# Optimization experiments

Hardware: AMD Instinct MI355X
Metric: run time of the kernel (lower is better)

## Reference

```python
import jax, jax.numpy as jnp
import numpy as np

SIGMA = 0.05  # gaussian bandwidth from the source


def _sqdist(a, b):
    # a: [B,N,D], b: [B,M,D] -> [B,N,M] squared euclidean distance
    a2 = jnp.sum(a * a, axis=-1)[:, :, None]
    b2 = jnp.sum(b * b, axis=-1)[:, None, :]
    return a2 + b2 - 2.0 * jnp.einsum('bnd,bmd->bnm', a, b)


def setup_inputs() -> dict:
    key = jax.random.key(0)
    k1, k2, k3, k4 = jax.random.split(key, 4)
    B, N, D = 2, 4096, 32
    points = jax.random.normal(k1, (B, N, 3), dtype=jnp.float32)
    pointfea1 = jax.random.normal(k2, (B, N, D), dtype=jnp.float32)
    pointfea2 = jax.random.normal(k3, (B, N, D), dtype=jnp.float32)
    weights = jax.random.uniform(k4, (B, N), dtype=jnp.float32) / N  # point-cloud mass weights
    return {"points": points, "pointfea1": pointfea1, "pointfea2": pointfea2, "weights": weights}


def reference(points, pointfea1, pointfea2, weights):
    # naive_corres: per-point spatial log-gaussian softmax vs feature log-softmax,
    # weighted squared difference, reduced over both pair axes -> [B]
    x = points / SIGMA
    point_loggauss = jax.nn.log_softmax(-_sqdist(x, x), axis=2)          # [B,N,N]
    fea_logsoftmax = jax.nn.log_softmax(-_sqdist(pointfea1, pointfea2), axis=2)  # [B,N,N]
    diff2 = (jnp.exp(point_loggauss) - jnp.exp(fea_logsoftmax)) ** 2
    l2_loss = jnp.sum(diff2 * weights[:, :, None], axis=2)  # sum over j
    return jnp.sum(l2_loss, axis=1)                          # sum over i -> [B]
```

## Files before the change

### kernel.cpp

```cpp
#include <hip/hip_runtime.h>

#define D    32
#define BLK  256
#define BLKP 64
#define NCH  16
#define SJ   128

#define LOG2E 1.44269504088896340736f

typedef short  short8  __attribute__((ext_vector_type(8)));
typedef float  floatx4 __attribute__((ext_vector_type(4)));
typedef float  v2f     __attribute__((ext_vector_type(2)));

__device__ __forceinline__ short f2bf(float v) {
    union { float f; unsigned u; } x; x.f = v;
    unsigned r = x.u + 0x7fffu + ((x.u >> 16) & 1u);
    return (short)(r >> 16);
}
__device__ __forceinline__ float bf2f(short h) {
    union { float f; unsigned u; } x;
    x.u = ((unsigned)(unsigned short)h) << 16;
    return x.f;
}
__device__ __forceinline__ float fast_exp2(float x) {
#if __has_builtin(__builtin_amdgcn_exp2f)
    return __builtin_amdgcn_exp2f(x);
#else
    return exp2f(x);
#endif
}

__global__ __launch_bounds__(BLKP) void precompute_kernel(
    const float* __restrict__ points,
    const float* __restrict__ fea1,
    const float* __restrict__ fea2,
    float4* __restrict__ xp,
    float* __restrict__ f1n,
    float* __restrict__ f2n,
    short* __restrict__ f2hi,
    short* __restrict__ f2lo,
    float* __restrict__ acc,
    float* __restrict__ out,
    int BN, int Bsz)
{
    int r = blockIdx.x * BLKP + threadIdx.x;
    if (r < Bsz) out[r] = 0.0f;
    if (r >= BN) return;
#pragma unroll
    for (int s = 0; s < 5; ++s) acc[s * BN + r] = 0.0f;

    const float s20 = 20.0f;
    float x = points[3*r+0] * s20;
    float y = points[3*r+1] * s20;
    float z = points[3*r+2] * s20;
    float4 v; v.x = x; v.y = y; v.z = z;
    v.w = (x*x + y*y + z*z) * LOG2E;
    xp[r] = v;

    const float4* p1 = (const float4*)(fea1 + (size_t)r * D);
    float n1 = 0.f;
#pragma unroll
    for (int k = 0; k < D/4; ++k) {
        float4 a = p1[k];
        n1 = fmaf(a.x,a.x, fmaf(a.y,a.y, fmaf(a.z,a.z, fmaf(a.w,a.w, n1))));
    }
    f1n[r] = n1 * LOG2E;

    const int t = r >> 4;
    const int m = r & 15;
    const float* p2 = fea2 + (size_t)r * D;
    float n2 = 0.f;
#pragma unroll
    for (int q = 0; q < 4; ++q) {
        float4 v0 = *(const float4*)(p2 + q*8);
        float4 v1 = *(const float4*)(p2 + q*8 + 4);
        float e[8] = {v0.x,v0.y,v0.z,v0.w,v1.x,v1.y,v1.z,v1.w};
        short8 h, l;
#pragma unroll
        for (int k = 0; k < 8; ++k) {
            n2 = fmaf(e[k], e[k], n2);
            short hh = f2bf(e[k]);
            h[k] = hh;
            l[k] = f2bf(e[k] - bf2f(hh));
        }
        size_t off = ((size_t)t * 64 + m + 16*q) * 8;
        *(short8*)&f2hi[off] = h;
        *(short8*)&f2lo[off] = l;
    }
    f2n[r] = n2 * LOG2E;
}

__global__ __launch_bounds__(BLK, 8) void pair_kernel(
    const float* __restrict__ fea1,
    const short* __restrict__ f2hi,
    const short* __restrict__ f2lo,
    const float4* __restrict__ xp,
    const float* __restrict__ f1n,
    const float* __restrict__ f2n,
    float* __restrict__ acc,
    int N, int BN)
{
    __shared__ __align__(16) short sHi[SJ * D];
    __shared__ __align__(16) short sLo[SJ * D];

    const int tid  = threadIdx.x;
    const int lane = tid & 63;
    const int wv   = tid >> 6;
    const int m    = lane & 15;
    const int q    = lane >> 4;

    const int ibpb  = N / 64;
    const int b     = blockIdx.x / ibpb;
    const int ibase = blockIdx.x * 64 + wv * 16;
    const int JCH   = N / NCH;
    const int jc0   = blockIdx.y * JCH;

    const float* f1p = fea1 + (size_t)(ibase + m) * D + q * 8;
    float4 bv0 = *(const float4*)(f1p);
    float4 bv1 = *(const float4*)(f1p + 4);
    float bf[8] = {bv0.x,bv0.y,bv0.z,bv0.w,bv1.x,bv1.y,bv1.z,bv1.w};
    short8 Bhi, Blo;
#pragma unroll
    for (int k = 0; k < 8; ++k) {
        short h = f2bf(bf[k]);
        Bhi[k] = h;
        Blo[k] = f2bf(bf[k] - bf2f(h));
    }

    const float L2 = 2.0f * LOG2E;
    float4 xi = xp[ibase + m];
    float xix = xi.x * L2, xiy = xi.y * L2, xiz = xi.z * L2;
    float mxiw = -xi.w;
    float nfi  = -f1n[ibase + m];

    v2f sAB = {0.f, 0.f};
    v2f s2  = {0.f, 0.f};
    float sab = 0.f;

    const short*  gHi  = f2hi + ((size_t)(b * N + jc0) >> 4) * 512;
    const short*  gLo  = f2lo + ((size_t)(b * N + jc0) >> 4) * 512;
    const float4* xpb  = xp  + (size_t)b * N + jc0;
    const float*  f2nb = f2n + (size_t)b * N + jc0;

    for (int s = 0; s < JCH; s += SJ) {
        const uint4* srcH = (const uint4*)(gHi + (size_t)(s >> 4) * 512);
        const uint4* srcL = (const uint4*)(gLo + (size_t)(s >> 4) * 512);
        uint4* dstH = (uint4*)sHi;
        uint4* dstL = (uint4*)sLo;
        dstH[tid]       = srcH[tid];
        dstH[tid + 256] = srcH[tid + 256];
        dstL[tid]       = srcL[tid];
        dstL[tid + 256] = srcL[tid + 256];
        __syncthreads();

        const float4* xps = xpb + s;
        const float*  fns = f2nb + s;

#pragma unroll 2
        for (int jt8 = 0; jt8 < SJ/16; ++jt8) {
            const short8 Ahi = *(const short8*)&sHi[(jt8 * 64 + lane) * 8];
            const short8 Alo = *(const short8*)&sLo[(jt8 * 64 + lane) * 8];
            floatx4 c = {0.f, 0.f, 0.f, 0.f};
            c = __builtin_amdgcn_mfma_f32_16x16x32_bf16(Ahi, Bhi, c, 0, 0, 0);
            c = __builtin_amdgcn_mfma_f32_16x16x32_bf16(Ahi, Blo, c, 0, 0, 0);
            c = __builtin_amdgcn_mfma_f32_16x16x32_bf16(Alo, Bhi, c, 0, 0, 0);
#pragma unroll
            for (int r = 0; r < 4; ++r) {
                int jl = jt8 * 16 + q * 4 + r;
                float4 xj = xps[jl];
                float bL = fmaf(c[r], L2, nfi - fns[jl]);
                float aL = fmaf(xiz, xj.z,
                             fmaf(xiy, xj.y,
                              fmaf(xix, xj.x, mxiw))) - xj.w;
                float ea = fast_exp2(aL);
                float eb = fast_exp2(bL);
                v2f e = {ea, eb};
                sAB += e;
                s2   = __builtin_elementwise_fma(e, e, s2);
                sab  = fmaf(ea, eb, sab);
            }
        }
        __syncthreads();
    }

    float vA = sAB.x, vB = sAB.y, v2a = s2.x, v2b = s2.y, vab = sab;
    vA  += __shfl_xor(vA, 16);  vA  += __shfl_xor(vA, 32);
    vB  += __shfl_xor(vB, 16);  vB  += __shfl_xor(vB, 32);
    v2a += __shfl_xor(v2a, 16); v2a += __shfl_xor(v2a, 32);
    v2b += __shfl_xor(v2b, 16); v2b += __shfl_xor(v2b, 32);
    vab += __shfl_xor(vab, 16); vab += __shfl_xor(vab, 32);

    if (lane < 16) {
        int row = ibase + lane;
        atomicAdd(&acc[0*BN + row], vA);
        atomicAdd(&acc[1*BN + row], v2a);
        atomicAdd(&acc[2*BN + row], vB);
        atomicAdd(&acc[3*BN + row], v2b);
        atomicAdd(&acc[4*BN + row], vab);
    }
}

__global__ __launch_bounds__(BLK) void finalize_kernel(
    const float* __restrict__ acc,
    const float* __restrict__ weights,
    float* __restrict__ out,
    int N, int BN)
{
    int row = blockIdx.x * BLK + threadIdx.x;
    int b   = (blockIdx.x * BLK) / N;

    float A   = acc[0*BN + row];
    float S2a = acc[1*BN + row];
    float Bt  = acc[2*BN + row];
    float S2b = acc[3*BN + row];
    float Sab = acc[4*BN + row];
    float invA = 1.0f / A;
    float invB = 1.0f / Bt;
    float val  = S2a*invA*invA - 2.0f*Sab*invA*invB + S2b*invB*invB;
    float sum  = weights[row] * val;

    __shared__ float red[BLK/64];
    for (int off = 32; off > 0; off >>= 1)
        sum += __shfl_down(sum, off);
    if ((threadIdx.x & 63) == 0) red[threadIdx.x >> 6] = sum;
    __syncthreads();
    if (threadIdx.x == 0) {
        float s = 0.f;
#pragma unroll
        for (int w = 0; w < BLK/64; ++w) s += red[w];
        atomicAdd(&out[b], s);
    }
}

extern "C" void kernel_launch(void* const* d_in, const int* in_sizes, int n_in,
                              void* d_out, int out_size, void* d_ws, size_t ws_size,
                              hipStream_t stream) {
    const float* points  = (const float*)d_in[0];
    const float* fea1    = (const float*)d_in[1];
    const float* fea2    = (const float*)d_in[2];
    const float* weights = (const float*)d_in[3];
    float* out = (float*)d_out;

    int B  = out_size;
    int BN = in_sizes[3];
    int N  = BN / B;

    float*  acc  = (float*)d_ws;
    float4* xp   = (float4*)((char*)d_ws + (size_t)5  * BN * 4);
    float*  f2n  = (float*)((char*)d_ws + (size_t)9  * BN * 4);
    float*  f1n  = (float*)((char*)d_ws + (size_t)10 * BN * 4);
    short*  f2hi = (short*)((char*)d_ws + (size_t)11 * BN * 4);
    short*  f2lo = f2hi + (size_t)BN * D;

    precompute_kernel<<<dim3((BN + BLKP - 1) / BLKP), dim3(BLKP), 0, stream>>>(
        points, fea1, fea2, xp, f1n, f2n, f2hi, f2lo, acc, out, BN, B);

    dim3 grid(BN / 64, NCH);
    pair_kernel<<<grid, dim3(BLK), 0, stream>>>(
        fea1, f2hi, f2lo, xp, f1n, f2n, acc, N, BN);

    finalize_kernel<<<dim3(BN / BLK), dim3(BLK), 0, stream>>>(acc, weights, out, N, BN);
}
```

Measured before the change: 92.29 us.

## Pack per-j point/norm data pairwise, stage in LDS, and use packed v2f math

Precompute now writes per-column x,y,z, negated squared norm and negated feature norm interleaved in pairs (12 floats per 2 columns). The pair kernel stages this into shared memory alongside the bf16 tiles. It then processes two columns at a time with 2-wide float vector FMAs, which can map to packed FP32 instructions. This replaces per-element global loads of xp and f2n inside the hot loop and halves the scalar FMA count, at the cost of extra LDS traffic and a sync-covered copy.

```diff
diff --git a/kernel.cpp b/kernel.cpp
--- a/kernel.cpp
+++ b/kernel.cpp
@@ -36,7 +36,7 @@
     const float* __restrict__ fea2,
     float4* __restrict__ xp,
     float* __restrict__ f1n,
-    float* __restrict__ f2n,
+    float* __restrict__ jpk,
     short* __restrict__ f2hi,
     short* __restrict__ f2lo,
     float* __restrict__ acc,
@@ -87,21 +87,28 @@
         *(short8*)&f2hi[off] = h;
         *(short8*)&f2lo[off] = l;
     }
-    f2n[r] = n2 * LOG2E;
+
+    float* jb = jpk + (size_t)(r >> 1) * 12 + (r & 1);
+    jb[0] = v.x;
+    jb[2] = v.y;
+    jb[4] = v.z;
+    jb[6] = -v.w;
+    jb[8] = -n2 * LOG2E;
 }
 
 __global__ __launch_bounds__(BLK, 8) void pair_kernel(
     const float* __restrict__ fea1,
     const short* __restrict__ f2hi,
     const short* __restrict__ f2lo,
+    const float* __restrict__ jpk,
     const float4* __restrict__ xp,
     const float* __restrict__ f1n,
-    const float* __restrict__ f2n,
     float* __restrict__ acc,
     int N, int BN)
 {
     __shared__ __align__(16) short sHi[SJ * D];
     __shared__ __align__(16) short sLo[SJ * D];
+    __shared__ __align__(16) float sJP[(SJ/2) * 12];
 
     const int tid  = threadIdx.x;
     const int lane = tid & 63;
@@ -129,32 +136,37 @@
 
     const float L2 = 2.0f * LOG2E;
     float4 xi = xp[ibase + m];
-    float xix = xi.x * L2, xiy = xi.y * L2, xiz = xi.z * L2;
-    float mxiw = -xi.w;
-    float nfi  = -f1n[ibase + m];
-
-    v2f sAB = {0.f, 0.f};
-    v2f s2  = {0.f, 0.f};
-    float sab = 0.f;
-
-    const short*  gHi  = f2hi + ((size_t)(b * N + jc0) >> 4) * 512;
-    const short*  gLo  = f2lo + ((size_t)(b * N + jc0) >> 4) * 512;
-    const float4* xpb  = xp  + (size_t)b * N + jc0;
-    const float*  f2nb = f2n + (size_t)b * N + jc0;
+    float nfi = -f1n[ibase + m];
+    v2f vxx2 = {xi.x * L2, xi.x * L2};
+    v2f vxy2 = {xi.y * L2, xi.y * L2};
+    v2f vxz2 = {xi.z * L2, xi.z * L2};
+    v2f vmw2 = {-xi.w, -xi.w};
+    v2f vnf2 = {nfi, nfi};
+    v2f vL2  = {L2, L2};
+
+    v2f sA2  = {0.f, 0.f};
+    v2f sB2  = {0.f, 0.f};
+    v2f s2a2 = {0.f, 0.f};
+    v2f s2b2 = {0.f, 0.f};
+    v2f sab2 = {0.f, 0.f};
+
+    const short* gHi = f2hi + ((size_t)(b * N + jc0) >> 4) * 512;
+    const short* gLo = f2lo + ((size_t)(b * N + jc0) >> 4) * 512;
+    const float* gJP = jpk  + ((size_t)(b * N + jc0) >> 1) * 12;
 
     for (int s = 0; s < JCH; s += SJ) {
         const uint4* srcH = (const uint4*)(gHi + (size_t)(s >> 4) * 512);
         const uint4* srcL = (const uint4*)(gLo + (size_t)(s >> 4) * 512);
+        const uint4* srcJ = (const uint4*)(gJP + (size_t)(s >> 1) * 12);
         uint4* dstH = (uint4*)sHi;
         uint4* dstL = (uint4*)sLo;
         dstH[tid]       = srcH[tid];
         dstH[tid + 256] = srcH[tid + 256];
         dstL[tid]       = srcL[tid];
         dstL[tid + 256] = srcL[tid + 256];
+        if (tid < (SJ/2) * 12 * 4 / 16)
+            ((uint4*)sJP)[tid] = srcJ[tid];
         __syncthreads();
-
-        const float4* xps = xpb + s;
-        const float*  fns = f2nb + s;
 
 #pragma unroll 2
         for (int jt8 = 0; jt8 < SJ/16; ++jt8) {
@@ -165,25 +177,39 @@
             c = __builtin_amdgcn_mfma_f32_16x16x32_bf16(Ahi, Blo, c, 0, 0, 0);
             c = __builtin_amdgcn_mfma_f32_16x16x32_bf16(Alo, Bhi, c, 0, 0, 0);
 #pragma unroll
-            for (int r = 0; r < 4; ++r) {
-                int jl = jt8 * 16 + q * 4 + r;
-                float4 xj = xps[jl];
-                float bL = fmaf(c[r], L2, nfi - fns[jl]);
-                float aL = fmaf(xiz, xj.z,
-                             fmaf(xiy, xj.y,
-                              fmaf(xix, xj.x, mxiw))) - xj.w;
-                float ea = fast_exp2(aL);
-                float eb = fast_exp2(bL);
-                v2f e = {ea, eb};
-                sAB += e;
-                s2   = __builtin_elementwise_fma(e, e, s2);
-                sab  = fmaf(ea, eb, sab);
+            for (int h = 0; h < 2; ++h) {
+                const int jp = jt8 * 8 + q * 2 + h;
+                float4 XY = *(const float4*)&sJP[jp * 12 + 0];
+                float4 ZW = *(const float4*)&sJP[jp * 12 + 4];
+                v2f    Fn = *(const v2f*)  &sJP[jp * 12 + 8];
+                v2f xx = {XY.x, XY.y};
+                v2f yy = {XY.z, XY.w};
+                v2f zz = {ZW.x, ZW.y};
+                v2f wn = {ZW.z, ZW.w};
+                v2f c2 = {c[2*h], c[2*h + 1]};
+                v2f t0 = __builtin_elementwise_fma(xx, vxx2, vmw2);
+                t0 = __builtin_elementwise_fma(yy, vxy2, t0);
+                t0 = __builtin_elementwise_fma(zz, vxz2, t0);
+                v2f aL = t0 + wn;
+                v2f bL = __builtin_elementwise_fma(c2, vL2, vnf2 + Fn);
+                v2f ea = {fast_exp2(aL.x), fast_exp2(aL.y)};
+                v2f eb = {fast_exp2(bL.x), fast_exp2(bL.y)};
+                sA2 += ea;
+                sB2 += eb;
+                s2a2 = __builtin_elementwise_fma(ea, ea, s2a2);
+                s2b2 = __builtin_elementwise_fma(eb, eb, s2b2);
+                sab2 = __builtin_elementwise_fma(ea, eb, sab2);
             }
         }
         __syncthreads();
     }
 
-    float vA = sAB.x, vB = sAB.y, v2a = s2.x, v2b = s2.y, vab = sab;
+    float vA  = sA2.x  + sA2.y;
+    float vB  = sB2.x  + sB2.y;
+    float v2a = s2a2.x + s2a2.y;
+    float v2b = s2b2.x + s2b2.y;
+    float vab = sab2.x + sab2.y;
+
     vA  += __shfl_xor(vA, 16);  vA  += __shfl_xor(vA, 32);
     vB  += __shfl_xor(vB, 16);  vB  += __shfl_xor(vB, 32);
     v2a += __shfl_xor(v2a, 16); v2a += __shfl_xor(v2a, 32);
@@ -247,17 +273,17 @@
 
     float*  acc  = (float*)d_ws;
     float4* xp   = (float4*)((char*)d_ws + (size_t)5  * BN * 4);
-    float*  f2n  = (float*)((char*)d_ws + (size_t)9  * BN * 4);
-    float*  f1n  = (float*)((char*)d_ws + (size_t)10 * BN * 4);
-    short*  f2hi = (short*)((char*)d_ws + (size_t)11 * BN * 4);
+    float*  f1n  = (float*)((char*)d_ws + (size_t)9  * BN * 4);
+    float*  jpk  = (float*)((char*)d_ws + (size_t)10 * BN * 4);
+    short*  f2hi = (short*)((char*)d_ws + (size_t)16 * BN * 4);
     short*  f2lo = f2hi + (size_t)BN * D;
 
     precompute_kernel<<<dim3((BN + BLKP - 1) / BLKP), dim3(BLKP), 0, stream>>>(
-        points, fea1, fea2, xp, f1n, f2n, f2hi, f2lo, acc, out, BN, B);
+        points, fea1, fea2, xp, f1n, jpk, f2hi, f2lo, acc, out, BN, B);
 
     dim3 grid(BN / 64, NCH);
     pair_kernel<<<grid, dim3(BLK), 0, stream>>>(
-        fea1, f2hi, f2lo, xp, f1n, f2n, acc, N, BN);
+        fea1, f2hi, f2lo, jpk, xp, f1n, acc, N, BN);
 
     finalize_kernel<<<dim3(BN / BLK), dim3(BLK), 0, stream>>>(acc, weights, out, N, BN);
 }
```

Result: faster. 82.48 us, median of 2 (-10.6%).
